# Optimization experiments

Measured on AMD Instinct MI355X. Metric: run time of the kernel, lower is better.

## Reference

```python
import jax, jax.numpy as jnp
import numpy as np

N_MEL = 80; ENC = 512; ARNN = 1024; DRNN = 1024; PRE = 256
ADIM = 128; NFILT = 32; KS = 31
B = 16; T_ENC = 128; T_DEC = 128
NEG = -1e30  # stand-in for -inf mask value


def _lstm_cell(x, h, c, wih, whh, bih, bhh):
    # PyTorch LSTMCell gate order: i, f, g, o
    gates = x @ wih.T + h @ whh.T + bih + bhh
    i, f, g, o = jnp.split(gates, 4, axis=-1)
    c = jax.nn.sigmoid(f) * c + jax.nn.sigmoid(i) * jnp.tanh(g)
    h = jax.nn.sigmoid(o) * jnp.tanh(c)
    return h, c


def _forward(memory, mels, memory_lengths, prenet_w1, prenet_w2,
             arnn_wih, arnn_whh, arnn_bih, arnn_bhh,
             query_w, memory_w, v_w, loc_conv_w, loc_dense_w,
             drnn_wih, drnn_whh, drnn_bih, drnn_bhh,
             proj_w, proj_b, gate_w, gate_b):
    bsz, t_enc, enc = memory.shape
    t_dec = mels.shape[2]
    valid = jnp.arange(t_enc)[None, :] < memory_lengths[:, None]  # [B,T_enc]
    proc_mem = memory @ memory_w.T  # [B,T_enc,ADIM], precomputed once

    # parse_decoder_inputs + go frame: use go frame + teacher frames 0..T-2
    teacher = jnp.transpose(mels, (2, 0, 1))  # [T_dec,B,n_mel]
    go = jnp.zeros((1, bsz, mels.shape[1]), mels.dtype)
    dec_in = jnp.concatenate([go, teacher], axis=0)[:t_dec]
    # Prenet (dropout is p=0.0 in source, so omitted)
    x = jax.nn.relu(dec_in @ prenet_w1.T)
    x = jax.nn.relu(x @ prenet_w2.T)  # [T_dec,B,PRE]

    pad = (KS - 1) // 2

    def step(carry, x_t):
        attn_h, attn_c, dec_h, dec_c, aw, awc, ctx = carry
        # attention RNN
        cell_in = jnp.concatenate([x_t, ctx], axis=-1)
        attn_h2, attn_c2 = _lstm_cell(cell_in, attn_h, attn_c,
                                      arnn_wih, arnn_whh, arnn_bih, arnn_bhh)
        # location-sensitive attention
        aw_cat = jnp.stack([aw, awc], axis=1)  # [B,2,T_enc]
        loc = jax.lax.conv_general_dilated(
            aw_cat, loc_conv_w, (1,), [(pad, pad)],
            dimension_numbers=('NCH', 'OIH', 'NCH'))  # [B,NFILT,T_enc]
        loc = jnp.einsum('bft,af->bta', loc, loc_dense_w)  # [B,T_enc,ADIM]
        pq = attn_h2 @ query_w.T  # [B,ADIM]
        e = jnp.tanh(pq[:, None, :] + loc + proc_mem) @ v_w[0]  # [B,T_enc]
        e = jnp.where(valid, e, NEG)
        aw2 = jax.nn.softmax(e, axis=1)
        ctx2 = jnp.einsum('bt,bte->be', aw2, memory)  # [B,ENC]
        awc2 = awc + aw2
        # decoder RNN
        dec_in2 = jnp.concatenate([attn_h2, ctx2], axis=-1)
        dec_h2, dec_c2 = _lstm_cell(dec_in2, dec_h, dec_c,
                                    drnn_wih, drnn_whh, drnn_bih, drnn_bhh)
        hc = jnp.concatenate([dec_h2, ctx2], axis=-1)
        mel = hc @ proj_w.T + proj_b      # [B,n_mel]
        gate = hc @ gate_w.T + gate_b     # [B,1]
        new_carry = (attn_h2, attn_c2, dec_h2, dec_c2, aw2, awc2, ctx2)
        return new_carry, (mel, gate[:, 0], aw2)

    z = lambda *s: jnp.zeros(s, memory.dtype)
    carry0 = (z(bsz, ARNN), z(bsz, ARNN), z(bsz, DRNN), z(bsz, DRNN),
              z(bsz, t_enc), z(bsz, t_enc), z(bsz, enc))
    _, (mels_out, gates, aligns) = jax.lax.scan(step, carry0, x)
    mel_outputs = jnp.transpose(mels_out, (1, 2, 0))   # [B,n_mel,T_dec]
    gate_outputs = jnp.transpose(gates, (1, 0))        # [B,T_dec]
    alignments = jnp.transpose(aligns, (1, 0, 2))      # [B,T_dec,T_enc]
    return mel_outputs, gate_outputs, alignments


def setup_inputs() -> dict:
    key = jax.random.key(0)
    ks = jax.random.split(key, 24)

    def g(i, shape):
        fan_in = shape[-1] if len(shape) <= 2 else int(np.prod(shape[1:]))
        return jax.random.normal(ks[i], shape, jnp.float32) / np.float32(np.sqrt(fan_in))

    return {
        'memory': jax.random.normal(ks[0], (B, T_ENC, ENC), jnp.float32),
        'mels': jax.random.normal(ks[1], (B, N_MEL, T_DEC), jnp.float32),
        'memory_lengths': jax.random.randint(ks[2], (B,), T_ENC // 2, T_ENC + 1),
        'prenet_w1': g(3, (PRE, N_MEL)),
        'prenet_w2': g(4, (PRE, PRE)),
        'arnn_wih': g(5, (4 * ARNN, PRE + ENC)),
        'arnn_whh': g(6, (4 * ARNN, ARNN)),
        'arnn_bih': g(7, (4 * ARNN,)),
        'arnn_bhh': g(8, (4 * ARNN,)),
        'query_w': g(9, (ADIM, ARNN)),
        'memory_w': g(10, (ADIM, ENC)),
        'v_w': g(11, (1, ADIM)),
        'loc_conv_w': g(12, (NFILT, 2, KS)),
        'loc_dense_w': g(13, (ADIM, NFILT)),
        'drnn_wih': g(14, (4 * DRNN, ARNN + ENC)),
        'drnn_whh': g(15, (4 * DRNN, DRNN)),
        'drnn_bih': g(16, (4 * DRNN,)),
        'drnn_bhh': g(17, (4 * DRNN,)),
        'proj_w': g(18, (N_MEL, DRNN + ENC)),
        'proj_b': g(19, (N_MEL,)),
        'gate_w': g(20, (1, DRNN + ENC)),
        'gate_b': g(21, (1,)),
    }


def reference(memory, mels, memory_lengths, prenet_w1, prenet_w2,
              arnn_wih, arnn_whh, arnn_bih, arnn_bhh,
              query_w, memory_w, v_w, loc_conv_w, loc_dense_w,
              drnn_wih, drnn_whh, drnn_bih, drnn_bhh,
              proj_w, proj_b, gate_w, gate_b):
    return _forward(memory, mels, memory_lengths, prenet_w1, prenet_w2,
                    arnn_wih, arnn_whh, arnn_bih, arnn_bhh,
                    query_w, memory_w, v_w, loc_conv_w, loc_dense_w,
                    drnn_wih, drnn_whh, drnn_bih, drnn_bhh,
                    proj_w, proj_b, gate_w, gate_b)
```

## Files before the change

### kernel.cpp

```cpp
#include <hip/hip_runtime.h>
#include <hip/hip_cooperative_groups.h>

namespace cg = cooperative_groups;

#define N_MEL 80
#define ENC   512
#define ARNN  1024
#define PRE   256
#define ADIM  128
#define NFILT 32
#define KS    31
#define BSZ   16
#define TENC  128
#define TDEC  128

#define OFF_XA     0u
#define OFF_X      8388608u
#define OFF_H1     8912896u
#define OFF_DECIN  9437184u
#define OFF_PM     9601024u
#define OFF_ATTNH  9863168u
#define OFF_DECH   9895936u
#define OFF_CTX    9928704u
#define OFF_CTR    9945088u
#define STATE_FLOATS 81984

__device__ __forceinline__ float sigmf(float x) { return 1.0f / (1.0f + __expf(-x)); }
__device__ __forceinline__ float tanhfast(float x) { return 1.0f - 2.0f / (__expf(2.0f * x) + 1.0f); }
__device__ __forceinline__ float dot4(const float4& w, const float4& x) {
    return w.x * x.x + w.y * x.y + w.z * x.z + w.w * x.w;
}

__device__ __forceinline__ void rel_add(unsigned* p) {
    __builtin_amdgcn_fence(__ATOMIC_RELEASE, "agent");
    __hip_atomic_fetch_add(p, 1u, __ATOMIC_RELAXED, __HIP_MEMORY_SCOPE_AGENT);
}
__device__ __forceinline__ void spin_until(unsigned* p, unsigned target) {
    while (__hip_atomic_load(p, __ATOMIC_RELAXED, __HIP_MEMORY_SCOPE_AGENT) < target)
        __builtin_amdgcn_s_sleep(2);
    __builtin_amdgcn_fence(__ATOMIC_ACQUIRE, "agent");
}


__global__ void __launch_bounds__(1024) build_decin(const float* __restrict__ mels,
                                                    float* __restrict__ decin) {
    int idx = blockIdx.x * 1024 + threadIdx.x;
    if (idx >= 128 * 16 * 80) return;
    int t = idx / 1280, r = idx % 1280;
    int b = r / 80, m = r % 80;
    decin[idx] = (t == 0) ? 0.f : mels[b * (80 * 128) + m * 128 + (t - 1)];
}

__global__ void __launch_bounds__(256) gemm_kernel(
    const float* __restrict__ A, int lda,
    const float* __restrict__ B, int ldb,
    float* __restrict__ C, int ldc,
    int M, int N, int K,
    const float* __restrict__ bias1, const float* __restrict__ bias2, int relu) {
    __shared__ float As[16][68];
    __shared__ float Bs[16][68];
    int tid = threadIdx.x;
    int tn = tid & 15, tm = tid >> 4;
    int m0 = blockIdx.y * 64, n0 = blockIdx.x * 64;
    float acc[4][4] = {};
    for (int k0 = 0; k0 < K; k0 += 16) {
        for (int idx = tid; idx < 1024; idx += 256) {
            int mm = idx >> 4, kk = idx & 15;
            int kg = k0 + kk;
            As[kk][mm] = (kg < K) ? A[(size_t)(m0 + mm) * lda + kg] : 0.f;
            Bs[kk][mm] = (kg < K) ? B[(size_t)(n0 + mm) * ldb + kg] : 0.f;
        }
        __syncthreads();
#pragma unroll
        for (int kk = 0; kk < 16; kk++) {
            float av[4], bv[4];
#pragma unroll
            for (int i = 0; i < 4; i++) { av[i] = As[kk][tm * 4 + i]; bv[i] = Bs[kk][tn * 4 + i]; }
#pragma unroll
            for (int i = 0; i < 4; i++)
#pragma unroll
                for (int j = 0; j < 4; j++) acc[i][j] += av[i] * bv[j];
        }
        __syncthreads();
    }
    for (int i = 0; i < 4; i++) {
        int m = m0 + tm * 4 + i;
        for (int j = 0; j < 4; j++) {
            int n = n0 + tn * 4 + j;
            float v = acc[i][j];
            if (bias1) v += bias1[n];
            if (bias2) v += bias2[n];
            if (relu) v = fmaxf(v, 0.f);
            C[(size_t)m * ldc + n] = v;
        }
    }
}


struct DecArgs {
    const float* memory;
    const int* memlen;
    const float* arnn_wih;
    const float* arnn_whh;
    const float* drnn_wih;
    const float* drnn_whh;
    const float* drnn_bih;
    const float* drnn_bhh;
    const float* query_w;
    const float* v_w;
    const float* conv_w;
    const float* dense_w;
    const float* proj_w;
    const float* proj_b;
    const float* gate_w;
    const float* gate_b;
    float* ws;
    float* out;
};

__global__ void __launch_bounds__(512, 2) decoder_main(DecArgs A) {
    cg::grid_group grid = cg::this_grid();
    const int tid = threadIdx.x;
    const int wv = tid >> 6;
    const int l = tid & 63;
    const int blk = blockIdx.x;
    const int u = wv & 3;
    const int kq = wv >> 2;
    const int jj = blk * 4 + u;
    const int col = kq * 256 + l * 4;
    float* ws = A.ws;
    unsigned* ctrA = (unsigned*)(ws + OFF_CTR);
    unsigned* ctrB = (unsigned*)(ws + OFF_CTR + 32);

    __shared__ float s_pm[128 * 132];
    __shared__ float s_loc[128 * 33];
    __shared__ float s_dw[128 * 33];
    __shared__ float s_cw[1984];
    __shared__ float s_ah[1024];
    __shared__ float s_ep[512];
    __shared__ float s_part[8][64];
    __shared__ float s_pq[128];
    __shared__ float s_ev[128];
    __shared__ float s_aw2[128];
    __shared__ float s_awl[128];
    __shared__ float s_awcl[128];
    __shared__ float s_attnc[64];
    __shared__ float s_decc[64];
    __shared__ float s_db[16];
    __shared__ float s_vw[128];
    __shared__ float s_red[2];

    {
        int g = blk * 512 + tid;
        if (g < STATE_FLOATS) ws[OFF_ATTNH + g] = 0.f;
    }
    if (tid < 128) { s_awl[tid] = 0.f; s_awcl[tid] = 0.f; }
    if (tid < 64) { s_attnc[tid] = 0.f; s_decc[tid] = 0.f; }
    if (tid < 16) {
        int uu = tid >> 2, gg = tid & 3;
        s_db[tid] = A.drnn_bih[gg * 1024 + blk * 4 + uu] + A.drnn_bhh[gg * 1024 + blk * 4 + uu];
    }
    if (tid < 128) s_vw[tid] = A.v_w[tid];
    for (int idx = tid; idx < 4096; idx += 512) {
        int a = idx >> 5, f = idx & 31;
        s_dw[a * 33 + f] = A.dense_w[idx];
    }
    if (blk < 16) {
        for (int idx = tid; idx < 16384; idx += 512) {
            int tt = idx >> 7, a = idx & 127;
            s_pm[tt * 132 + a] = ws[OFF_PM + (blk * 128 + tt) * 128 + a];
        }
        for (int idx = tid; idx < 1984; idx += 512) s_cw[idx] = A.conv_w[idx];
    }
    const int ml = (blk < 16) ? A.memlen[blk] : 0;

    float4 wA[12];
    {
#pragma unroll
        for (int g = 0; g < 4; g++)
            wA[g] = *reinterpret_cast<const float4*>(
                A.arnn_wih + (size_t)(g * 1024 + jj) * 768 + 256 + col);
#pragma unroll
        for (int ch = 1; ch < 3; ch++)
#pragma unroll
            for (int g = 0; g < 4; g++)
                wA[ch * 4 + g] = *reinterpret_cast<const float4*>(
                    A.arnn_whh + (size_t)(g * 1024 + jj) * 1024 + (ch - 1) * 512 + col);
    }
    float4 wD[20];
    {
#pragma unroll
        for (int ch = 0; ch < 3; ch++)
#pragma unroll
            for (int g = 0; g < 4; g++)
                wD[ch * 4 + g] = *reinterpret_cast<const float4*>(
                    A.drnn_wih + (size_t)(g * 1024 + jj) * 1536 + ch * 512 + col);
#pragma unroll
        for (int ch = 3; ch < 5; ch++)
#pragma unroll
            for (int g = 0; g < 4; g++)
                wD[ch * 4 + g] = *reinterpret_cast<const float4*>(
                    A.drnn_whh + (size_t)(g * 1024 + jj) * 1024 + (ch - 3) * 512 + col);
    }
    __syncthreads();
    grid.sync();

    auto reduce4 = [&](float p0, float p1, float p2, float p3) -> float {
        float a01 = (l & 1) ? p1 : p0;
        float b01 = (l & 1) ? p0 : p1;
        a01 += __shfl_xor(b01, 1);
        float a23 = (l & 1) ? p3 : p2;
        float b23 = (l & 1) ? p2 : p3;
        a23 += __shfl_xor(b23, 1);
        float k_ = (l & 2) ? a23 : a01;
        float s_ = (l & 2) ? a01 : a23;
        k_ += __shfl_xor(s_, 2);
        k_ += __shfl_xor(k_, 4);
        k_ += __shfl_xor(k_, 8);
        k_ += __shfl_xor(k_, 16);
        k_ += __shfl_xor(k_, 32);
        return k_;
    };

    auto attn_stage = [&](int t, int wpar, int rpar) {
        const float* hb = ws + OFF_ATTNH + rpar * 16384;
        const float* cb = ws + OFF_CTX + rpar * 8192;
        float xa0 = 0.f, xa1 = 0.f, xa2 = 0.f, xa3 = 0.f;
        if (tid < 64) {
            int eb = tid & 15, eu = tid >> 4;
            const float* xa = ws + OFF_XA + (size_t)(t * 16 + eb) * 4096 + (blk * 4 + eu);
            xa0 = xa[0]; xa1 = xa[1024]; xa2 = xa[2048]; xa3 = xa[3072];
        }
#pragma unroll 4
        for (int b = 0; b < 16; b++) {
            float4 x0 = *reinterpret_cast<const float4*>(cb + b * 512 + col);
            float4 x1 = *reinterpret_cast<const float4*>(hb + b * 1024 + col);
            float4 x2 = *reinterpret_cast<const float4*>(hb + b * 1024 + 512 + col);
            float p0 = dot4(wA[0], x0) + dot4(wA[4], x1) + dot4(wA[8], x2);
            float p1 = dot4(wA[1], x0) + dot4(wA[5], x1) + dot4(wA[9], x2);
            float p2 = dot4(wA[2], x0) + dot4(wA[6], x1) + dot4(wA[10], x2);
            float p3 = dot4(wA[3], x0) + dot4(wA[7], x1) + dot4(wA[11], x2);
            float r = reduce4(p0, p1, p2, p3);
            if (l < 4) s_part[wv][b * 4 + l] = r;
        }
        __syncthreads();
        if (tid < 64) {
            int eu = tid >> 4, eb = tid & 15;
            float G0 = s_part[eu][eb * 4 + 0] + s_part[eu + 4][eb * 4 + 0] + xa0;
            float G1 = s_part[eu][eb * 4 + 1] + s_part[eu + 4][eb * 4 + 1] + xa1;
            float G2 = s_part[eu][eb * 4 + 2] + s_part[eu + 4][eb * 4 + 2] + xa2;
            float G3 = s_part[eu][eb * 4 + 3] + s_part[eu + 4][eb * 4 + 3] + xa3;
            float ig = sigmf(G0), fg = sigmf(G1), gg = tanhfast(G2), og = sigmf(G3);
            float c = fg * s_attnc[tid] + ig * gg;
            s_attnc[tid] = c;
            ws[OFF_ATTNH + wpar * 16384 + eb * 1024 + blk * 4 + eu] = og * tanhfast(c);
        }
    };

    auto dec_stage = [&](int wpar, int rpar) {
        const float* hb = ws + OFF_ATTNH + wpar * 16384;
        const float* cb = ws + OFF_CTX + wpar * 8192;
        const float* db = ws + OFF_DECH + rpar * 16384;
#pragma unroll 2
        for (int b = 0; b < 16; b++) {
            float4 x0 = *reinterpret_cast<const float4*>(hb + b * 1024 + col);
            float4 x1 = *reinterpret_cast<const float4*>(hb + b * 1024 + 512 + col);
            float4 x2 = *reinterpret_cast<const float4*>(cb + b * 512 + col);
            float4 x3 = *reinterpret_cast<const float4*>(db + b * 1024 + col);
            float4 x4 = *reinterpret_cast<const float4*>(db + b * 1024 + 512 + col);
            float p0 = dot4(wD[0], x0) + dot4(wD[4], x1) + dot4(wD[8], x2) + dot4(wD[12], x3) + dot4(wD[16], x4);
            float p1 = dot4(wD[1], x0) + dot4(wD[5], x1) + dot4(wD[9], x2) + dot4(wD[13], x3) + dot4(wD[17], x4);
            float p2 = dot4(wD[2], x0) + dot4(wD[6], x1) + dot4(wD[10], x2) + dot4(wD[14], x3) + dot4(wD[18], x4);
            float p3 = dot4(wD[3], x0) + dot4(wD[7], x1) + dot4(wD[11], x2) + dot4(wD[15], x3) + dot4(wD[19], x4);
            float r = reduce4(p0, p1, p2, p3);
            if (l < 4) s_part[wv][b * 4 + l] = r;
        }
        __syncthreads();
        if (tid < 64) {
            int eu = tid >> 4, eb = tid & 15;
            float G0 = s_part[eu][eb * 4 + 0] + s_part[eu + 4][eb * 4 + 0] + s_db[eu * 4 + 0];
            float G1 = s_part[eu][eb * 4 + 1] + s_part[eu + 4][eb * 4 + 1] + s_db[eu * 4 + 1];
            float G2 = s_part[eu][eb * 4 + 2] + s_part[eu + 4][eb * 4 + 2] + s_db[eu * 4 + 2];
            float G3 = s_part[eu][eb * 4 + 3] + s_part[eu + 4][eb * 4 + 3] + s_db[eu * 4 + 3];
            float ig = sigmf(G0), fg = sigmf(G1), gg = tanhfast(G2), og = sigmf(G3);
            float c = fg * s_decc[tid] + ig * gg;
            s_decc[tid] = c;
            ws[OFF_DECH + wpar * 16384 + eb * 1024 + blk * 4 + eu] = og * tanhfast(c);
        }
        __syncthreads();
    };

    auto attention = [&](int t, int wpar) {
        const int b = blk;
        s_ah[tid] = ws[OFF_ATTNH + wpar * 16384 + b * 1024 + tid];
        s_ah[tid + 512] = ws[OFF_ATTNH + wpar * 16384 + b * 1024 + 512 + tid];
        __syncthreads();
        for (int idx = tid; idx < 4096; idx += 512) {
            int f = idx >> 7, tt = idx & 127;
            const float* w0 = s_cw + f * 62;
            float s = 0.f;
#pragma unroll
            for (int k = 0; k < 31; k++) {
                int j = tt + k - 15;
                if (j >= 0 && j < 128) s += w0[k] * s_awl[j] + w0[31 + k] * s_awcl[j];
            }
            s_loc[tt * 33 + f] = s;
        }
#pragma unroll 2
        for (int ii = 0; ii < 16; ii++) {
            int a = wv * 16 + ii;
            const float* qw = A.query_w + a * 1024;
            float s = 0.f;
#pragma unroll
            for (int q = 0; q < 4; q++) {
                int k = q * 256 + l * 4;
                float4 h4 = *reinterpret_cast<const float4*>(&s_ah[k]);
                float4 w4 = *reinterpret_cast<const float4*>(&qw[k]);
                s += dot4(w4, h4);
            }
#pragma unroll
            for (int off = 1; off < 64; off <<= 1) s += __shfl_xor(s, off);
            if (l == 0) s_pq[a] = s;
        }
        __syncthreads();
        {
            int tt = tid >> 2, sl = tid & 3;
            float part = 0.f;
            for (int i = 0; i < 32; i++) {
                int a = i * 4 + sl;
                float lp = 0.f;
#pragma unroll
                for (int f = 0; f < 32; f++) lp += s_loc[tt * 33 + f] * s_dw[a * 33 + f];
                float arg = s_pq[a] + lp + s_pm[tt * 132 + a];
                part += s_vw[a] * tanhfast(arg);
            }
            s_ep[tid] = part;
        }
        __syncthreads();
        if (tid < 128) {
            float s = s_ep[tid * 4] + s_ep[tid * 4 + 1] + s_ep[tid * 4 + 2] + s_ep[tid * 4 + 3];
            if (tid >= ml) s = -1e30f;
            s_ev[tid] = s;
        }
        __syncthreads();
        if (wv == 0) {
            float m = fmaxf(s_ev[l], s_ev[l + 64]);
#pragma unroll
            for (int off = 1; off < 64; off <<= 1) m = fmaxf(m, __shfl_xor(m, off));
            if (l == 0) s_red[0] = m;
        }
        __syncthreads();
        if (tid < 128) s_aw2[tid] = __expf(s_ev[tid] - s_red[0]);
        __syncthreads();
        if (wv == 0) {
            float s = s_aw2[l] + s_aw2[l + 64];
#pragma unroll
            for (int off = 1; off < 64; off <<= 1) s += __shfl_xor(s, off);
            if (l == 0) s_red[1] = 1.f / s;
        }
        __syncthreads();
        if (tid < 128) {
            float val = s_aw2[tid] * s_red[1];
            s_aw2[tid] = val;
            s_awl[tid] = val;
            s_awcl[tid] += val;
            A.out[165888 + b * 16384 + t * 128 + tid] = val;
        }
        __syncthreads();
        {
            const float* mb = A.memory + (size_t)b * 65536 + tid;
            float acc = 0.f;
#pragma unroll 8
            for (int tt2 = 0; tt2 < 128; tt2++) acc += s_aw2[tt2] * mb[tt2 * 512];
            ws[OFF_CTX + wpar * 8192 + b * 512 + tid] = acc;
        }
    };

    auto eout = [&](int tdone) {
        int widx = (blk - 16) * 8 + wv;
        if (widx >= 1296) return;
        int ppar = tdone & 1;
        int b; const float* wrow; float bias; float* dst;
        if (widx < 1280) {
            b = widx / 80; int m = widx % 80;
            wrow = A.proj_w + m * 1536; bias = A.proj_b[m];
            dst = A.out + (size_t)(b * 80 + m) * 128 + tdone;
        } else {
            b = widx - 1280;
            wrow = A.gate_w; bias = A.gate_b[0];
            dst = A.out + 163840 + b * 128 + tdone;
        }
        const float* h1p = ws + OFF_DECH + ppar * 16384 + b * 1024;
        const float* c1p = ws + OFF_CTX + ppar * 8192 + b * 512;
        float s = 0.f;
#pragma unroll
        for (int q = 0; q < 6; q++) {
            int k = q * 256 + l * 4;
            float4 w4 = *reinterpret_cast<const float4*>(&wrow[k]);
            float4 h4;
            if (k < 1024) h4 = *reinterpret_cast<const float4*>(&h1p[k]);
            else h4 = *reinterpret_cast<const float4*>(&c1p[k - 1024]);
            s += dot4(w4, h4);
        }
#pragma unroll
        for (int off = 1; off < 64; off <<= 1) s += __shfl_xor(s, off);
        if (l == 0) *dst = s + bias;
    };

    for (int t = 0; t < 128; t++) {
        int wpar = t & 1, rpar = wpar ^ 1;
        attn_stage(t, wpar, rpar);
        __syncthreads();
        if (tid == 0) rel_add(ctrA);
        if (blk < 16) {
            if (tid == 0) spin_until(ctrA, 256u * (unsigned)(t + 1));
            __syncthreads();
            attention(t, wpar);
            __syncthreads();
            if (tid == 0) { rel_add(ctrB); spin_until(ctrB, 16u * (unsigned)(t + 1)); }
            __syncthreads();
        } else {
            if (tid == 0) spin_until(ctrB, 16u * (unsigned)(t + 1));
            __syncthreads();
            if (t >= 1) eout(t - 1);
        }
        dec_stage(wpar, rpar);
    }
    if (tid == 0) rel_add(ctrA);
    if (blk >= 16) {
        if (tid == 0) spin_until(ctrA, 256u * 129u);
        __syncthreads();
        eout(127);
    }
}


extern "C" void kernel_launch(void* const* d_in, const int* in_sizes, int n_in,
                              void* d_out, int out_size, void* d_ws, size_t ws_size,
                              hipStream_t stream) {
    (void)in_sizes; (void)n_in; (void)out_size; (void)ws_size;
    const float* memory    = (const float*)d_in[0];
    const float* mels      = (const float*)d_in[1];
    const int*   memlen    = (const int*)d_in[2];
    const float* prenet_w1 = (const float*)d_in[3];
    const float* prenet_w2 = (const float*)d_in[4];
    const float* arnn_wih  = (const float*)d_in[5];
    const float* arnn_whh  = (const float*)d_in[6];
    const float* arnn_bih  = (const float*)d_in[7];
    const float* arnn_bhh  = (const float*)d_in[8];
    const float* query_w   = (const float*)d_in[9];
    const float* memory_w  = (const float*)d_in[10];
    const float* v_w       = (const float*)d_in[11];
    const float* conv_w    = (const float*)d_in[12];
    const float* dense_w   = (const float*)d_in[13];
    const float* drnn_wih  = (const float*)d_in[14];
    const float* drnn_whh  = (const float*)d_in[15];
    const float* drnn_bih  = (const float*)d_in[16];
    const float* drnn_bhh  = (const float*)d_in[17];
    const float* proj_w    = (const float*)d_in[18];
    const float* proj_b    = (const float*)d_in[19];
    const float* gate_w    = (const float*)d_in[20];
    const float* gate_b    = (const float*)d_in[21];
    float* ws = (float*)d_ws;
    float* out = (float*)d_out;

    build_decin<<<dim3(160), dim3(1024), 0, stream>>>(mels, ws + OFF_DECIN);
    gemm_kernel<<<dim3(4, 32), dim3(256), 0, stream>>>(ws + OFF_DECIN, 80, prenet_w1, 80,
                                                       ws + OFF_H1, 256, 2048, 256, 80,
                                                       nullptr, nullptr, 1);
    gemm_kernel<<<dim3(4, 32), dim3(256), 0, stream>>>(ws + OFF_H1, 256, prenet_w2, 256,
                                                       ws + OFF_X, 256, 2048, 256, 256,
                                                       nullptr, nullptr, 1);
    gemm_kernel<<<dim3(64, 32), dim3(256), 0, stream>>>(ws + OFF_X, 256, arnn_wih, 768,
                                                        ws + OFF_XA, 4096, 2048, 4096, 256,
                                                        arnn_bih, arnn_bhh, 0);
    gemm_kernel<<<dim3(2, 32), dim3(256), 0, stream>>>(memory, 512, memory_w, 512,
                                                       ws + OFF_PM, 128, 2048, 128, 512,
                                                       nullptr, nullptr, 0);

    DecArgs a;
    a.memory = memory; a.memlen = memlen;
    a.arnn_wih = arnn_wih; a.arnn_whh = arnn_whh;
    a.drnn_wih = drnn_wih; a.drnn_whh = drnn_whh;
    a.drnn_bih = drnn_bih; a.drnn_bhh = drnn_bhh;
    a.query_w = query_w; a.v_w = v_w;
    a.conv_w = conv_w; a.dense_w = dense_w;
    a.proj_w = proj_w; a.proj_b = proj_b;
    a.gate_w = gate_w; a.gate_b = gate_b;
    a.ws = ws; a.out = out;
    void* kargs[] = { &a };
    hipLaunchCooperativeKernel((const void*)decoder_main, dim3(256), dim3(512),
                               kargs, 0, stream);
}
```

Before: 12.09 ms.

## Replace fences with volatile loads and hierarchical counters for grid sync

Drops the agent-scope release/acquire fences around the cross-block counters. Cross-block state reads and writes now go through volatile accesses, and an explicit vmcnt wait precedes each counter increment. The 256-block arrive counter becomes 16 sub-counters of 16 blocks each, so only the last arriver in a group bumps the global counter, which cuts atomic contention. The eout-side blocks now also wait on the attention-RNN barrier before projecting the previous step. Without real fences, correctness rests on volatile (cache-bypassing) accesses, which is a memory-ordering risk.

```diff
diff --git a/kernel.cpp b/kernel.cpp
--- a/kernel.cpp
+++ b/kernel.cpp
@@ -23,22 +23,27 @@
 #define OFF_DECH   9895936u
 #define OFF_CTX    9928704u
 #define OFF_CTR    9945088u
-#define STATE_FLOATS 81984
+#define STATE_FLOATS 82496
+
+typedef float vf4 __attribute__((ext_vector_type(4)));
 
 __device__ __forceinline__ float sigmf(float x) { return 1.0f / (1.0f + __expf(-x)); }
 __device__ __forceinline__ float tanhfast(float x) { return 1.0f - 2.0f / (__expf(2.0f * x) + 1.0f); }
-__device__ __forceinline__ float dot4(const float4& w, const float4& x) {
+__device__ __forceinline__ float dot4(const float4& w, const vf4& x) {
     return w.x * x.x + w.y * x.y + w.z * x.z + w.w * x.w;
 }
-
-__device__ __forceinline__ void rel_add(unsigned* p) {
-    __builtin_amdgcn_fence(__ATOMIC_RELEASE, "agent");
-    __hip_atomic_fetch_add(p, 1u, __ATOMIC_RELAXED, __HIP_MEMORY_SCOPE_AGENT);
-}
-__device__ __forceinline__ void spin_until(unsigned* p, unsigned target) {
-    while (__hip_atomic_load(p, __ATOMIC_RELAXED, __HIP_MEMORY_SCOPE_AGENT) < target)
-        __builtin_amdgcn_s_sleep(2);
-    __builtin_amdgcn_fence(__ATOMIC_ACQUIRE, "agent");
+__device__ __forceinline__ float dot4f(const float4& w, const float4& x) {
+    return w.x * x.x + w.y * x.y + w.z * x.z + w.w * x.w;
+}
+
+__device__ __forceinline__ vf4 vload4(const float* p) { return *(const volatile vf4*)p; }
+__device__ __forceinline__ float vloadf(const float* p) { return *(const volatile float*)p; }
+__device__ __forceinline__ void vstoref(float* p, float v) { *(volatile float*)p = v; }
+
+__device__ __forceinline__ void wait_ge(unsigned* p, unsigned tgt) {
+    while (__hip_atomic_load(p, __ATOMIC_RELAXED, __HIP_MEMORY_SCOPE_AGENT) < tgt)
+        __builtin_amdgcn_s_sleep(1);
+    asm volatile("" ::: "memory");
 }
 
 
@@ -131,6 +136,8 @@
     float* ws = A.ws;
     unsigned* ctrA = (unsigned*)(ws + OFF_CTR);
     unsigned* ctrB = (unsigned*)(ws + OFF_CTR + 32);
+    const int grp = blk >> 4;
+    unsigned* subA = (unsigned*)(ws + OFF_CTR + 64 + grp * 32);
 
     __shared__ float s_pm[128 * 132];
     __shared__ float s_loc[128 * 33];
@@ -233,9 +240,9 @@
         }
 #pragma unroll 4
         for (int b = 0; b < 16; b++) {
-            float4 x0 = *reinterpret_cast<const float4*>(cb + b * 512 + col);
-            float4 x1 = *reinterpret_cast<const float4*>(hb + b * 1024 + col);
-            float4 x2 = *reinterpret_cast<const float4*>(hb + b * 1024 + 512 + col);
+            vf4 x0 = vload4(cb + b * 512 + col);
+            vf4 x1 = vload4(hb + b * 1024 + col);
+            vf4 x2 = vload4(hb + b * 1024 + 512 + col);
             float p0 = dot4(wA[0], x0) + dot4(wA[4], x1) + dot4(wA[8], x2);
             float p1 = dot4(wA[1], x0) + dot4(wA[5], x1) + dot4(wA[9], x2);
             float p2 = dot4(wA[2], x0) + dot4(wA[6], x1) + dot4(wA[10], x2);
@@ -253,7 +260,7 @@
             float ig = sigmf(G0), fg = sigmf(G1), gg = tanhfast(G2), og = sigmf(G3);
             float c = fg * s_attnc[tid] + ig * gg;
             s_attnc[tid] = c;
-            ws[OFF_ATTNH + wpar * 16384 + eb * 1024 + blk * 4 + eu] = og * tanhfast(c);
+            vstoref(ws + OFF_ATTNH + wpar * 16384 + eb * 1024 + blk * 4 + eu, og * tanhfast(c));
         }
     };
 
@@ -263,11 +270,11 @@
         const float* db = ws + OFF_DECH + rpar * 16384;
 #pragma unroll 2
         for (int b = 0; b < 16; b++) {
-            float4 x0 = *reinterpret_cast<const float4*>(hb + b * 1024 + col);
-            float4 x1 = *reinterpret_cast<const float4*>(hb + b * 1024 + 512 + col);
-            float4 x2 = *reinterpret_cast<const float4*>(cb + b * 512 + col);
-            float4 x3 = *reinterpret_cast<const float4*>(db + b * 1024 + col);
-            float4 x4 = *reinterpret_cast<const float4*>(db + b * 1024 + 512 + col);
+            vf4 x0 = vload4(hb + b * 1024 + col);
+            vf4 x1 = vload4(hb + b * 1024 + 512 + col);
+            vf4 x2 = vload4(cb + b * 512 + col);
+            vf4 x3 = vload4(db + b * 1024 + col);
+            vf4 x4 = vload4(db + b * 1024 + 512 + col);
             float p0 = dot4(wD[0], x0) + dot4(wD[4], x1) + dot4(wD[8], x2) + dot4(wD[12], x3) + dot4(wD[16], x4);
             float p1 = dot4(wD[1], x0) + dot4(wD[5], x1) + dot4(wD[9], x2) + dot4(wD[13], x3) + dot4(wD[17], x4);
             float p2 = dot4(wD[2], x0) + dot4(wD[6], x1) + dot4(wD[10], x2) + dot4(wD[14], x3) + dot4(wD[18], x4);
@@ -285,15 +292,15 @@
             float ig = sigmf(G0), fg = sigmf(G1), gg = tanhfast(G2), og = sigmf(G3);
             float c = fg * s_decc[tid] + ig * gg;
             s_decc[tid] = c;
-            ws[OFF_DECH + wpar * 16384 + eb * 1024 + blk * 4 + eu] = og * tanhfast(c);
+            vstoref(ws + OFF_DECH + wpar * 16384 + eb * 1024 + blk * 4 + eu, og * tanhfast(c));
         }
         __syncthreads();
     };
 
     auto attention = [&](int t, int wpar) {
         const int b = blk;
-        s_ah[tid] = ws[OFF_ATTNH + wpar * 16384 + b * 1024 + tid];
-        s_ah[tid + 512] = ws[OFF_ATTNH + wpar * 16384 + b * 1024 + 512 + tid];
+        s_ah[tid] = vloadf(ws + OFF_ATTNH + wpar * 16384 + b * 1024 + tid);
+        s_ah[tid + 512] = vloadf(ws + OFF_ATTNH + wpar * 16384 + b * 1024 + 512 + tid);
         __syncthreads();
         for (int idx = tid; idx < 4096; idx += 512) {
             int f = idx >> 7, tt = idx & 127;
@@ -316,7 +323,7 @@
                 int k = q * 256 + l * 4;
                 float4 h4 = *reinterpret_cast<const float4*>(&s_ah[k]);
                 float4 w4 = *reinterpret_cast<const float4*>(&qw[k]);
-                s += dot4(w4, h4);
+                s += dot4f(w4, h4);
             }
 #pragma unroll
             for (int off = 1; off < 64; off <<= 1) s += __shfl_xor(s, off);
@@ -372,7 +379,7 @@
             float acc = 0.f;
 #pragma unroll 8
             for (int tt2 = 0; tt2 < 128; tt2++) acc += s_aw2[tt2] * mb[tt2 * 512];
-            ws[OFF_CTX + wpar * 8192 + b * 512 + tid] = acc;
+            vstoref(ws + OFF_CTX + wpar * 8192 + b * 512 + tid, acc);
         }
     };
 
@@ -397,9 +404,9 @@
         for (int q = 0; q < 6; q++) {
             int k = q * 256 + l * 4;
             float4 w4 = *reinterpret_cast<const float4*>(&wrow[k]);
-            float4 h4;
-            if (k < 1024) h4 = *reinterpret_cast<const float4*>(&h1p[k]);
-            else h4 = *reinterpret_cast<const float4*>(&c1p[k - 1024]);
+            vf4 h4;
+            if (k < 1024) h4 = vload4(h1p + k);
+            else h4 = vload4(c1p + k - 1024);
             s += dot4(w4, h4);
         }
 #pragma unroll
@@ -411,24 +418,44 @@
         int wpar = t & 1, rpar = wpar ^ 1;
         attn_stage(t, wpar, rpar);
         __syncthreads();
-        if (tid == 0) rel_add(ctrA);
+        if (tid == 0) {
+            asm volatile("s_waitcnt vmcnt(0)" ::: "memory");
+            unsigned old = __hip_atomic_fetch_add(subA, 1u, __ATOMIC_RELAXED,
+                                                  __HIP_MEMORY_SCOPE_AGENT);
+            if (old == 16u * (unsigned)(t + 1) - 1u)
+                __hip_atomic_fetch_add(ctrA, 1u, __ATOMIC_RELAXED,
+                                       __HIP_MEMORY_SCOPE_AGENT);
+        }
         if (blk < 16) {
-            if (tid == 0) spin_until(ctrA, 256u * (unsigned)(t + 1));
+            if (tid == 0) wait_ge(ctrA, 16u * (unsigned)(t + 1));
             __syncthreads();
             attention(t, wpar);
             __syncthreads();
-            if (tid == 0) { rel_add(ctrB); spin_until(ctrB, 16u * (unsigned)(t + 1)); }
+            if (tid == 0) {
+                asm volatile("s_waitcnt vmcnt(0)" ::: "memory");
+                __hip_atomic_fetch_add(ctrB, 1u, __ATOMIC_RELAXED,
+                                       __HIP_MEMORY_SCOPE_AGENT);
+                wait_ge(ctrB, 16u * (unsigned)(t + 1));
+            }
             __syncthreads();
         } else {
-            if (tid == 0) spin_until(ctrB, 16u * (unsigned)(t + 1));
+            if (tid == 0) wait_ge(ctrA, 16u * (unsigned)(t + 1));
             __syncthreads();
             if (t >= 1) eout(t - 1);
+            if (tid == 0) wait_ge(ctrB, 16u * (unsigned)(t + 1));
+            __syncthreads();
         }
         dec_stage(wpar, rpar);
     }
-    if (tid == 0) rel_add(ctrA);
+    if (tid == 0) {
+        asm volatile("s_waitcnt vmcnt(0)" ::: "memory");
+        unsigned old = __hip_atomic_fetch_add(subA, 1u, __ATOMIC_RELAXED,
+                                              __HIP_MEMORY_SCOPE_AGENT);
+        if (old == 16u * 129u - 1u)
+            __hip_atomic_fetch_add(ctrA, 1u, __ATOMIC_RELAXED, __HIP_MEMORY_SCOPE_AGENT);
+    }
     if (blk >= 16) {
-        if (tid == 0) spin_until(ctrA, 256u * 129u);
+        if (tid == 0) wait_ge(ctrA, 16u * 129u);
         __syncthreads();
         eout(127);
     }
```

After: 12.63 ms. +4.5%, slower.
